# Performance work log

Hardware: AMD Instinct MI355X
Metric: run time of the kernel (lower is better)

The kernel has to match this reference:

```python
import jax, jax.numpy as jnp
import numpy as np

LN_EPS = 1e-5  # torch LayerNorm default

def _lnorm(x):
    # LayerNorm over last dim, no affine params
    mu = jnp.mean(x, axis=-1, keepdims=True)
    var = jnp.var(x, axis=-1, keepdims=True)
    return (x - mu) / jnp.sqrt(var + LN_EPS)

def setup_inputs() -> dict:
    key = jax.random.key(0)
    k0, k1, k2, k3 = jax.random.split(key, 4)
    B, S, D, H = 4, 4096, 1024, 64
    xs_q = jax.random.normal(k0, (B, S, D), dtype=jnp.float32)
    # torch Linear(D, H, bias=False) stores weight [H, D]; we store [D, H] = W.T
    sc = 1.0 / np.sqrt(D)
    Wq = jax.random.normal(k1, (D, H), dtype=jnp.float32) * sc
    Wk = jax.random.normal(k2, (D, H), dtype=jnp.float32) * sc
    Wv = jax.random.normal(k3, (D, H), dtype=jnp.float32) * sc
    return {"xs_q": xs_q, "Wq": Wq, "Wk": Wk, "Wv": Wv}

def reference(xs_q, Wq, Wk, Wv):
    # self-attention: xs_k_v = xs_q
    qs = _lnorm(jnp.einsum('bsd,dh->bsh', xs_q, Wq))  # [B,S,H]
    ks = _lnorm(jnp.einsum('bsd,dh->bsh', xs_q, Wk))
    vs = jnp.einsum('bsd,dh->bsh', xs_q, Wv)
    scaling = 1.0 / jnp.sqrt(jnp.asarray(qs.shape[-1], dtype=qs.dtype))
    att = jnp.einsum('bqh,bkh->bqk', qs, ks)          # [B,S,S] full attention matrix
    probs = jax.nn.softmax(scaling * att, axis=-1)
    vsp = jnp.einsum('bqk,bkh->bqh', probs, vs)       # [B,S,H]
    return vsp
```

## Files before the change

### kernel.cpp

```cpp
#include <hip/hip_runtime.h>
#include <hip/hip_bf16.h>


typedef __bf16 bf16x8 __attribute__((ext_vector_type(8)));
typedef __bf16 bf16x4 __attribute__((ext_vector_type(4)));
typedef float f32x4 __attribute__((ext_vector_type(4)));

#define NROW 16384
#define DD   1024
#define HH   64
#define SS   4096
#define LS   68

static __device__ inline unsigned short f2bf_u(float x) {
  __bf16 b = (__bf16)x;
  return __builtin_bit_cast(unsigned short, b);
}
static __device__ inline uint2 pk4f(float a, float b, float c, float d) {
  return make_uint2((unsigned)f2bf_u(a) | ((unsigned)f2bf_u(b) << 16),
                    (unsigned)f2bf_u(c) | ((unsigned)f2bf_u(d) << 16));
}
static __device__ inline bf16x8 ld8(const __bf16* p) {
  bf16x4 lo = *reinterpret_cast<const bf16x4*>(p);
  bf16x4 hi = *reinterpret_cast<const bf16x4*>(p + 4);
  return __builtin_shufflevector(lo, hi, 0, 1, 2, 3, 4, 5, 6, 7);
}

__global__ __launch_bounds__(256) void k_transpose_w(
    const float* __restrict__ Wq, const float* __restrict__ Wk,
    const float* __restrict__ Wv, __bf16* __restrict__ WT) {
  int idx = blockIdx.x * 256 + threadIdx.x;
  int mat = idx >> 16;
  int rem = idx & 65535;
  int k = rem >> 6, h = rem & 63;
  const float* W = (mat == 0) ? Wq : ((mat == 1) ? Wk : Wv);
  WT[(size_t)(mat * 64 + h) * DD + k] = (__bf16)W[rem];
}

__global__ __launch_bounds__(128, 2) void k_proj(
    const float* __restrict__ X, const __bf16* __restrict__ WT,
    __bf16* __restrict__ qb, __bf16* __restrict__ kbp, __bf16* __restrict__ vT) {
  __shared__ __bf16 Xs[32 * LS];
  __shared__ __bf16 Ws[192 * LS];
  const int t = threadIdx.x, lane = t & 63, w = t >> 6;
  const int quad = lane >> 4, m = lane & 15;
  const int Mb = blockIdx.x * 32;

  f32x4 acc[12];
#pragma unroll
  for (int i = 0; i < 12; i++) acc[i] = (f32x4){0.f, 0.f, 0.f, 0.f};

  float4 xr[4];
  bf16x8 wr[12];
#pragma unroll
  for (int i = 0; i < 4; i++) {
    int c = t + i * 128, row = c >> 4, col = (c & 15) * 4;
    xr[i] = *reinterpret_cast<const float4*>(&X[(size_t)(Mb + row) * DD + col]);
  }
#pragma unroll
  for (int i = 0; i < 12; i++) {
    int c = t + i * 128, row = c >> 3, col = (c & 7) * 8;
    wr[i] = *reinterpret_cast<const bf16x8*>(&WT[(size_t)row * DD + col]);
  }

  for (int s = 0; s < 16; s++) {
    if (s) __syncthreads();
#pragma unroll
    for (int i = 0; i < 4; i++) {
      int c = t + i * 128, row = c >> 4, col = (c & 15) * 4;
      *reinterpret_cast<uint2*>(&Xs[row * LS + col]) =
          pk4f(xr[i].x, xr[i].y, xr[i].z, xr[i].w);
    }
#pragma unroll
    for (int i = 0; i < 12; i++) {
      int c = t + i * 128, row = c >> 3, col = (c & 7) * 8;
      uint4 raw = __builtin_bit_cast(uint4, wr[i]);
      __bf16* wd = &Ws[row * LS + col];
      *reinterpret_cast<uint2*>(wd) = make_uint2(raw.x, raw.y);
      *reinterpret_cast<uint2*>(wd + 4) = make_uint2(raw.z, raw.w);
    }
    __syncthreads();
    if (s + 1 < 16) {
      const int ko = (s + 1) * 64;
#pragma unroll
      for (int i = 0; i < 4; i++) {
        int c = t + i * 128, row = c >> 4, col = (c & 15) * 4;
        xr[i] = *reinterpret_cast<const float4*>(
            &X[(size_t)(Mb + row) * DD + ko + col]);
      }
#pragma unroll
      for (int i = 0; i < 12; i++) {
        int c = t + i * 128, row = c >> 3, col = (c & 7) * 8;
        wr[i] = *reinterpret_cast<const bf16x8*>(
            &WT[(size_t)row * DD + ko + col]);
      }
    }
#pragma unroll
    for (int kk = 0; kk < 2; kk++) {
      bf16x8 a = ld8(&Xs[(16 * w + m) * LS + 32 * kk + quad * 8]);
#pragma unroll
      for (int nt = 0; nt < 12; nt++) {
        bf16x8 bfr = ld8(&Ws[(16 * nt + m) * LS + 32 * kk + quad * 8]);
        acc[nt] = __builtin_amdgcn_mfma_f32_16x16x32_bf16(a, bfr, acc[nt], 0, 0, 0);
      }
    }
  }

#pragma unroll
  for (int mat = 0; mat < 2; mat++) {
#pragma unroll
    for (int reg = 0; reg < 4; reg++) {
      float s = 0.f, s2 = 0.f;
#pragma unroll
      for (int ntl = 0; ntl < 4; ntl++) {
        float x = acc[mat * 4 + ntl][reg];
        s += x; s2 += x * x;
      }
#pragma unroll
      for (int off = 1; off < 16; off <<= 1) {
        s += __shfl_xor(s, off, 64);
        s2 += __shfl_xor(s2, off, 64);
      }
      float mu = s * (1.0f / 64.0f);
      float var = s2 * (1.0f / 64.0f) - mu * mu;
      float rstd = rsqrtf(var + 1e-5f);
      float scl = (mat == 0) ? 0.125f * 1.44269504f * rstd : rstd;
#pragma unroll
      for (int ntl = 0; ntl < 4; ntl++)
        acc[mat * 4 + ntl][reg] = (acc[mat * 4 + ntl][reg] - mu) * scl;
    }
  }

  const int rowbase = Mb + 16 * w + quad * 4;
#pragma unroll
  for (int nt = 0; nt < 4; nt++)
#pragma unroll
    for (int reg = 0; reg < 4; reg++) {
      qb[(size_t)(rowbase + reg) * HH + m + 16 * nt] = (__bf16)acc[nt][reg];
      kbp[(size_t)(rowbase + reg) * HH + m + 16 * nt] = (__bf16)acc[4 + nt][reg];
    }
  const int b = Mb >> 12;
  const int s0 = (Mb & 4095) + 16 * w + quad * 4;
#pragma unroll
  for (int nt = 0; nt < 4; nt++) {
    ushort4 pk = make_ushort4(f2bf_u(acc[8 + nt][0]), f2bf_u(acc[8 + nt][1]),
                              f2bf_u(acc[8 + nt][2]), f2bf_u(acc[8 + nt][3]));
    *reinterpret_cast<ushort4*>(
        &vT[((size_t)(b * 64) + m + 16 * nt) * SS + s0]) = pk;
  }
}

__global__ __launch_bounds__(256, 6) void k_attn(
    const __bf16* __restrict__ qb, const __bf16* __restrict__ kbp,
    const __bf16* __restrict__ vT, float* __restrict__ Op,
    float* __restrict__ lp, int spbits) {
  __shared__ __bf16 Klds[64 * LS];
  __shared__ __bf16 Vlds[64 * LS];
  __shared__ __bf16 Plds[4][16 * LS];
  const int t = threadIdx.x, lane = t & 63, w = t >> 6;
  const int quad = lane >> 4, m = lane & 15;
  const int nsp = 1 << spbits;
  const int qt = blockIdx.x >> spbits, sp = blockIdx.x & (nsp - 1);
  const int KPS = SS >> spbits;
  const int Mb = qt * 64;
  const int b = Mb >> 12;
  const size_t kvbase = (size_t)b * SS * HH;

  bf16x8 qf[2];
  {
    const int row = Mb + 16 * w + m;
    qf[0] = *reinterpret_cast<const bf16x8*>(&qb[(size_t)row * HH + quad * 8]);
    qf[1] = *reinterpret_cast<const bf16x8*>(&qb[(size_t)row * HH + 32 + quad * 8]);
  }
  bf16x8 ones;
#pragma unroll
  for (int i = 0; i < 8; i++) ones[i] = (__bf16)1.0f;

  f32x4 O[4], lac;
#pragma unroll
  for (int i = 0; i < 4; i++) O[i] = (f32x4){0.f, 0.f, 0.f, 0.f};
  lac = (f32x4){0.f, 0.f, 0.f, 0.f};

  const int c0row = t >> 3, ck0 = (t & 7) * 8;
  const int c1row = c0row + 32;
  const int kb_lo = sp * KPS, kb_hi = kb_lo + KPS;

  uint4 kd0, kd1, vd0, vd1;
  {
    kd0 = *reinterpret_cast<const uint4*>(&kbp[kvbase + (size_t)(kb_lo + c0row) * HH + ck0]);
    kd1 = *reinterpret_cast<const uint4*>(&kbp[kvbase + (size_t)(kb_lo + c1row) * HH + ck0]);
    vd0 = *reinterpret_cast<const uint4*>(&vT[(size_t)(b * 64 + c0row) * SS + kb_lo + ck0]);
    vd1 = *reinterpret_cast<const uint4*>(&vT[(size_t)(b * 64 + c1row) * SS + kb_lo + ck0]);
  }

  for (int kb0 = kb_lo; kb0 < kb_hi; kb0 += 64) {
    {
      __bf16* kp0 = &Klds[c0row * LS + ck0];
      __bf16* kp1 = &Klds[c1row * LS + ck0];
      __bf16* vp0 = &Vlds[c0row * LS + ck0];
      __bf16* vp1 = &Vlds[c1row * LS + ck0];
      *reinterpret_cast<uint2*>(kp0) = make_uint2(kd0.x, kd0.y);
      *reinterpret_cast<uint2*>(kp0 + 4) = make_uint2(kd0.z, kd0.w);
      *reinterpret_cast<uint2*>(kp1) = make_uint2(kd1.x, kd1.y);
      *reinterpret_cast<uint2*>(kp1 + 4) = make_uint2(kd1.z, kd1.w);
      *reinterpret_cast<uint2*>(vp0) = make_uint2(vd0.x, vd0.y);
      *reinterpret_cast<uint2*>(vp0 + 4) = make_uint2(vd0.z, vd0.w);
      *reinterpret_cast<uint2*>(vp1) = make_uint2(vd1.x, vd1.y);
      *reinterpret_cast<uint2*>(vp1 + 4) = make_uint2(vd1.z, vd1.w);
    }
    __syncthreads();
    if (kb0 + 64 < kb_hi) {
      kd0 = *reinterpret_cast<const uint4*>(&kbp[kvbase + (size_t)(kb0 + 64 + c0row) * HH + ck0]);
      kd1 = *reinterpret_cast<const uint4*>(&kbp[kvbase + (size_t)(kb0 + 64 + c1row) * HH + ck0]);
      vd0 = *reinterpret_cast<const uint4*>(&vT[(size_t)(b * 64 + c0row) * SS + kb0 + 64 + ck0]);
      vd1 = *reinterpret_cast<const uint4*>(&vT[(size_t)(b * 64 + c1row) * SS + kb0 + 64 + ck0]);
    }

    f32x4 sc[4];
#pragma unroll
    for (int nt = 0; nt < 4; nt++) sc[nt] = (f32x4){0.f, 0.f, 0.f, 0.f};
#pragma unroll
    for (int kk = 0; kk < 2; kk++)
#pragma unroll
      for (int nt = 0; nt < 4; nt++) {
        bf16x8 bf = ld8(&Klds[(m + 16 * nt) * LS + 32 * kk + quad * 8]);
        sc[nt] = __builtin_amdgcn_mfma_f32_16x16x32_bf16(qf[kk], bf, sc[nt], 0, 0, 0);
      }

    __bf16* Pw = Plds[w];
#pragma unroll
    for (int nt = 0; nt < 4; nt++)
#pragma unroll
      for (int reg = 0; reg < 4; reg++)
        Pw[(quad * 4 + reg) * LS + m + 16 * nt] = (__bf16)exp2f(sc[nt][reg]);

#pragma unroll
    for (int kk = 0; kk < 2; kk++) {
      bf16x8 pf = ld8(&Pw[m * LS + 32 * kk + quad * 8]);
      lac = __builtin_amdgcn_mfma_f32_16x16x32_bf16(ones, pf, lac, 0, 0, 0);
#pragma unroll
      for (int ht = 0; ht < 4; ht++) {
        bf16x8 vf = ld8(&Vlds[(m + 16 * ht) * LS + 32 * kk + quad * 8]);
        O[ht] = __builtin_amdgcn_mfma_f32_16x16x32_bf16(vf, pf, O[ht], 0, 0, 0);
      }
    }
    __syncthreads();
  }

  const int rowg = Mb + 16 * w + m;
  float4* obase = reinterpret_cast<float4*>(
      &Op[((size_t)sp * NROW + rowg) * HH + quad * 16]);
#pragma unroll
  for (int ht = 0; ht < 4; ht++)
    obase[ht] = make_float4(O[ht][0], O[ht][1], O[ht][2], O[ht][3]);
  if (quad == 0) lp[sp * NROW + rowg] = lac[0];
}

__global__ __launch_bounds__(256) void k_comb(const float* __restrict__ Op,
                                              const float* __restrict__ lp,
                                              float* __restrict__ out, int nsp) {
  int idx = blockIdx.x * 256 + threadIdx.x;
  int row = idx >> 6, h = idx & 63;
  int soff = ((h >> 2) & 3) * 16 + (h >> 4) * 4 + (h & 3);
  size_t sbase = (size_t)row * HH + soff;
  float o = 0.f, l = 0.f;
  for (int j = 0; j < nsp; j++) {
    o += Op[(size_t)j * NROW * HH + sbase];
    l += lp[j * NROW + row];
  }
  out[idx] = o / l;
}

extern "C" void kernel_launch(void* const* d_in, const int* in_sizes, int n_in,
                              void* d_out, int out_size, void* d_ws, size_t ws_size,
                              hipStream_t stream) {
  const float* X  = (const float*)d_in[0];
  const float* Wq = (const float*)d_in[1];
  const float* Wk = (const float*)d_in[2];
  const float* Wv = (const float*)d_in[3];
  float* out = (float*)d_out;
  char* ws = (char*)d_ws;

  __bf16* WT  = (__bf16*)(ws);
  __bf16* qb  = (__bf16*)(ws + (size_t)512 * 1024);
  __bf16* kbp = (__bf16*)(ws + (size_t)2560 * 1024);
  __bf16* vT  = (__bf16*)(ws + (size_t)4608 * 1024);
  float*  Op  = (float*)(ws + (size_t)6656 * 1024);
  const size_t need8 = (size_t)(6656 + 8 * 4096 + 512) * 1024;
  const int spbits = (ws_size >= need8) ? 3 : 2;
  const int nsp = 1 << spbits;
  float* lp = (float*)(ws + (size_t)(6656 + nsp * 4096) * 1024);

  hipLaunchKernelGGL(k_transpose_w, dim3(768), dim3(256), 0, stream, Wq, Wk, Wv, WT);
  hipLaunchKernelGGL(k_proj, dim3(NROW / 32), dim3(128), 0, stream, X, WT, qb, kbp, vT);
  hipLaunchKernelGGL(k_attn, dim3((NROW / 64) * nsp), dim3(256), 0, stream,
                     qb, kbp, vT, Op, lp, spbits);
  hipLaunchKernelGGL(k_comb, dim3(NROW * HH / 256), dim3(256), 0, stream,
                     Op, lp, out, nsp);
}
```

Measured before the change: 164.1 us.

## Keep P in registers via transposed S=K·Q tiles and split keys across waves

```diff
diff --git a/kernel.cpp b/kernel.cpp
--- a/kernel.cpp
+++ b/kernel.cpp
@@ -4,6 +4,7 @@
 
 typedef __bf16 bf16x8 __attribute__((ext_vector_type(8)));
 typedef __bf16 bf16x4 __attribute__((ext_vector_type(4)));
+typedef short s16x4 __attribute__((ext_vector_type(4)));
 typedef float f32x4 __attribute__((ext_vector_type(4)));
 
 #define NROW 16384
@@ -11,6 +12,16 @@
 #define HH   64
 #define SS   4096
 #define LS   68
+
+#if __has_builtin(__builtin_amdgcn_mfma_f32_16x16x16_bf16)
+#define MFMA16(a, b, c) __builtin_amdgcn_mfma_f32_16x16x16_bf16((a), (b), (c), 0, 0, 0)
+#define HAVE_MFMA16 1
+#elif __has_builtin(__builtin_amdgcn_mfma_f32_16x16x16bf16_1k)
+#define MFMA16(a, b, c)                                             \
+  __builtin_amdgcn_mfma_f32_16x16x16bf16_1k(                        \
+      __builtin_bit_cast(s16x4, (a)), __builtin_bit_cast(s16x4, (b)), (c), 0, 0, 0)
+#define HAVE_MFMA16 1
+#endif
 
 static __device__ inline unsigned short f2bf_u(float x) {
   __bf16 b = (__bf16)x;
@@ -150,15 +161,16 @@
   }
 }
 
-__global__ __launch_bounds__(256, 6) void k_attn(
+__global__ __launch_bounds__(256, 4) void k_attn(
     const __bf16* __restrict__ qb, const __bf16* __restrict__ kbp,
     const __bf16* __restrict__ vT, float* __restrict__ Op,
     float* __restrict__ lp, int spbits) {
-  __shared__ __bf16 Klds[64 * LS];
-  __shared__ __bf16 Vlds[64 * LS];
-  __shared__ __bf16 Plds[4][16 * LS];
+  __shared__ __align__(16) char smem[17408];
+  __bf16* Klds = (__bf16*)smem;
+  __bf16* Vlds = (__bf16*)(smem + 8704);
   const int t = threadIdx.x, lane = t & 63, w = t >> 6;
   const int quad = lane >> 4, m = lane & 15;
+  const int wq = w >> 1, wk = w & 1;
   const int nsp = 1 << spbits;
   const int qt = blockIdx.x >> spbits, sp = blockIdx.x & (nsp - 1);
   const int KPS = SS >> spbits;
@@ -166,32 +178,30 @@
   const int b = Mb >> 12;
   const size_t kvbase = (size_t)b * SS * HH;
 
-  bf16x8 qf[2];
-  {
-    const int row = Mb + 16 * w + m;
-    qf[0] = *reinterpret_cast<const bf16x8*>(&qb[(size_t)row * HH + quad * 8]);
-    qf[1] = *reinterpret_cast<const bf16x8*>(&qb[(size_t)row * HH + 32 + quad * 8]);
-  }
-  bf16x8 ones;
-#pragma unroll
-  for (int i = 0; i < 8; i++) ones[i] = (__bf16)1.0f;
-
-  f32x4 O[4], lac;
-#pragma unroll
-  for (int i = 0; i < 4; i++) O[i] = (f32x4){0.f, 0.f, 0.f, 0.f};
-  lac = (f32x4){0.f, 0.f, 0.f, 0.f};
+  bf16x8 qf[2][2];
+#pragma unroll
+  for (int ntl = 0; ntl < 2; ntl++)
+#pragma unroll
+    for (int kk = 0; kk < 2; kk++)
+      qf[ntl][kk] = *reinterpret_cast<const bf16x8*>(
+          &qb[(size_t)(Mb + (2 * wq + ntl) * 16 + m) * HH + 32 * kk + quad * 8]);
+
+  f32x4 O[4][2];
+#pragma unroll
+  for (int i = 0; i < 4; i++)
+#pragma unroll
+    for (int j = 0; j < 2; j++) O[i][j] = (f32x4){0.f, 0.f, 0.f, 0.f};
+  float ll[2] = {0.f, 0.f};
 
   const int c0row = t >> 3, ck0 = (t & 7) * 8;
   const int c1row = c0row + 32;
   const int kb_lo = sp * KPS, kb_hi = kb_lo + KPS;
 
   uint4 kd0, kd1, vd0, vd1;
-  {
-    kd0 = *reinterpret_cast<const uint4*>(&kbp[kvbase + (size_t)(kb_lo + c0row) * HH + ck0]);
-    kd1 = *reinterpret_cast<const uint4*>(&kbp[kvbase + (size_t)(kb_lo + c1row) * HH + ck0]);
-    vd0 = *reinterpret_cast<const uint4*>(&vT[(size_t)(b * 64 + c0row) * SS + kb_lo + ck0]);
-    vd1 = *reinterpret_cast<const uint4*>(&vT[(size_t)(b * 64 + c1row) * SS + kb_lo + ck0]);
-  }
+  kd0 = *reinterpret_cast<const uint4*>(&kbp[kvbase + (size_t)(kb_lo + c0row) * HH + ck0]);
+  kd1 = *reinterpret_cast<const uint4*>(&kbp[kvbase + (size_t)(kb_lo + c1row) * HH + ck0]);
+  vd0 = *reinterpret_cast<const uint4*>(&vT[(size_t)(b * 64 + c0row) * SS + kb_lo + ck0]);
+  vd1 = *reinterpret_cast<const uint4*>(&vT[(size_t)(b * 64 + c1row) * SS + kb_lo + ck0]);
 
   for (int kb0 = kb_lo; kb0 < kb_hi; kb0 += 64) {
     {
@@ -216,56 +226,112 @@
       vd1 = *reinterpret_cast<const uint4*>(&vT[(size_t)(b * 64 + c1row) * SS + kb0 + 64 + ck0]);
     }
 
-    f32x4 sc[4];
-#pragma unroll
-    for (int nt = 0; nt < 4; nt++) sc[nt] = (f32x4){0.f, 0.f, 0.f, 0.f};
-#pragma unroll
-    for (int kk = 0; kk < 2; kk++)
-#pragma unroll
-      for (int nt = 0; nt < 4; nt++) {
-        bf16x8 bf = ld8(&Klds[(m + 16 * nt) * LS + 32 * kk + quad * 8]);
-        sc[nt] = __builtin_amdgcn_mfma_f32_16x16x32_bf16(qf[kk], bf, sc[nt], 0, 0, 0);
-      }
-
-    __bf16* Pw = Plds[w];
-#pragma unroll
-    for (int nt = 0; nt < 4; nt++)
-#pragma unroll
-      for (int reg = 0; reg < 4; reg++)
-        Pw[(quad * 4 + reg) * LS + m + 16 * nt] = (__bf16)exp2f(sc[nt][reg]);
-
-#pragma unroll
-    for (int kk = 0; kk < 2; kk++) {
-      bf16x8 pf = ld8(&Pw[m * LS + 32 * kk + quad * 8]);
-      lac = __builtin_amdgcn_mfma_f32_16x16x32_bf16(ones, pf, lac, 0, 0, 0);
+#pragma unroll
+    for (int ktl = 0; ktl < 2; ktl++) {
+      const int kt = 2 * wk + ktl;
+      f32x4 sc[2];
+      sc[0] = (f32x4){0.f, 0.f, 0.f, 0.f};
+      sc[1] = (f32x4){0.f, 0.f, 0.f, 0.f};
+#pragma unroll
+      for (int kk = 0; kk < 2; kk++) {
+        bf16x8 kf = ld8(&Klds[(kt * 16 + m) * LS + 32 * kk + quad * 8]);
+        sc[0] = __builtin_amdgcn_mfma_f32_16x16x32_bf16(kf, qf[0][kk], sc[0], 0, 0, 0);
+        sc[1] = __builtin_amdgcn_mfma_f32_16x16x32_bf16(kf, qf[1][kk], sc[1], 0, 0, 0);
+      }
+#pragma unroll
+      for (int ntl = 0; ntl < 2; ntl++) {
+        float p0 = exp2f(sc[ntl][0]), p1 = exp2f(sc[ntl][1]);
+        float p2 = exp2f(sc[ntl][2]), p3 = exp2f(sc[ntl][3]);
+        ll[ntl] += (p0 + p1) + (p2 + p3);
+        bf16x4 pf;
+        pf[0] = (__bf16)p0; pf[1] = (__bf16)p1;
+        pf[2] = (__bf16)p2; pf[3] = (__bf16)p3;
+#ifdef HAVE_MFMA16
+#pragma unroll
+        for (int ht = 0; ht < 4; ht++) {
+          bf16x4 vf = *reinterpret_cast<const bf16x4*>(
+              &Vlds[(16 * ht + m) * LS + kt * 16 + quad * 4]);
+          O[ht][ntl] = MFMA16(vf, pf, O[ht][ntl]);
+        }
+#else
+        uint2 pd = __builtin_bit_cast(uint2, pf);
+        int lo_src = 32 * quad + m, hi_src = 32 * quad + 16 + m;
+        unsigned b0 = (unsigned)__shfl((int)pd.x, lo_src, 64);
+        unsigned b1 = (unsigned)__shfl((int)pd.y, lo_src, 64);
+        unsigned b2 = (unsigned)__shfl((int)pd.x, hi_src, 64);
+        unsigned b3 = (unsigned)__shfl((int)pd.y, hi_src, 64);
+        uint4 bz = (quad < 2) ? make_uint4(b0, b1, b2, b3)
+                              : make_uint4(0u, 0u, 0u, 0u);
+        bf16x8 bfrag = __builtin_bit_cast(bf16x8, bz);
+#pragma unroll
+        for (int ht = 0; ht < 4; ht++) {
+          bf16x8 vf = ld8(&Vlds[(16 * ht + m) * LS + kt * 16 + (quad & 1) * 8]);
+          O[ht][ntl] =
+              __builtin_amdgcn_mfma_f32_16x16x32_bf16(vf, bfrag, O[ht][ntl], 0, 0, 0);
+        }
+#endif
+      }
+    }
+    __syncthreads();
+  }
+
+#pragma unroll
+  for (int ntl = 0; ntl < 2; ntl++) {
+    ll[ntl] += __shfl_xor(ll[ntl], 16, 64);
+    ll[ntl] += __shfl_xor(ll[ntl], 32, 64);
+  }
+
+  float* obuf = (float*)smem;
+  float* lbuf = (float*)(smem + 16896);
+  __syncthreads();
+  if (wk == 1) {
+#pragma unroll
+    for (int ht = 0; ht < 4; ht++)
+#pragma unroll
+      for (int ntl = 0; ntl < 2; ntl++)
+#pragma unroll
+        for (int reg = 0; reg < 4; reg++)
+          obuf[wq * 2112 + (16 * ht + quad * 4 + reg) * 33 + ntl * 16 + m] =
+              O[ht][ntl][reg];
+    if (quad == 0) {
+      lbuf[(2 * wq + 0) * 16 + m] = ll[0];
+      lbuf[(2 * wq + 1) * 16 + m] = ll[1];
+    }
+  }
+  __syncthreads();
+  if (wk == 0) {
+#pragma unroll
+    for (int ht = 0; ht < 4; ht++)
+#pragma unroll
+      for (int ntl = 0; ntl < 2; ntl++)
+#pragma unroll
+        for (int reg = 0; reg < 4; reg++)
+          O[ht][ntl][reg] +=
+              obuf[wq * 2112 + (16 * ht + quad * 4 + reg) * 33 + ntl * 16 + m];
+#pragma unroll
+    for (int ntl = 0; ntl < 2; ntl++) {
+      const int qg = Mb + (2 * wq + ntl) * 16 + m;
+      ll[ntl] += lbuf[(2 * wq + ntl) * 16 + m];
 #pragma unroll
       for (int ht = 0; ht < 4; ht++) {
-        bf16x8 vf = ld8(&Vlds[(m + 16 * ht) * LS + 32 * kk + quad * 8]);
-        O[ht] = __builtin_amdgcn_mfma_f32_16x16x32_bf16(vf, pf, O[ht], 0, 0, 0);
-      }
-    }
-    __syncthreads();
-  }
-
-  const int rowg = Mb + 16 * w + m;
-  float4* obase = reinterpret_cast<float4*>(
-      &Op[((size_t)sp * NROW + rowg) * HH + quad * 16]);
-#pragma unroll
-  for (int ht = 0; ht < 4; ht++)
-    obase[ht] = make_float4(O[ht][0], O[ht][1], O[ht][2], O[ht][3]);
-  if (quad == 0) lp[sp * NROW + rowg] = lac[0];
+        f32x4 v = O[ht][ntl];
+        *reinterpret_cast<float4*>(
+            &Op[((size_t)sp * NROW + qg) * HH + 16 * ht + 4 * quad]) =
+            make_float4(v[0], v[1], v[2], v[3]);
+      }
+      if (quad == 0) lp[sp * NROW + qg] = ll[ntl];
+    }
+  }
 }
 
 __global__ __launch_bounds__(256) void k_comb(const float* __restrict__ Op,
                                               const float* __restrict__ lp,
                                               float* __restrict__ out, int nsp) {
   int idx = blockIdx.x * 256 + threadIdx.x;
-  int row = idx >> 6, h = idx & 63;
-  int soff = ((h >> 2) & 3) * 16 + (h >> 4) * 4 + (h & 3);
-  size_t sbase = (size_t)row * HH + soff;
+  int row = idx >> 6;
   float o = 0.f, l = 0.f;
   for (int j = 0; j < nsp; j++) {
-    o += Op[(size_t)j * NROW * HH + sbase];
+    o += Op[(size_t)j * NROW * HH + idx];
     l += lp[j * NROW + row];
   }
   out[idx] = o / l;
```

Measured after the change: 160.8 us. -2.0%, faster.
